# Performance work log

Hardware: AMD Instinct MI355X
Metric: run time of the kernel (lower is better)

The kernel has to match this reference:

```python
import jax, jax.numpy as jnp
import numpy as np

Q = 1024      # query length
R = 2048      # relative position length (2*Q, mems=None)
B = 2         # batch
D_MODEL = 1024
N_HEAD = 16
D_HEAD = 64
SCALE = 1.0 / (D_HEAD ** 0.5)
LN_EPS = 1e-12


def setup_inputs() -> dict:
    key = jax.random.key(0)
    ks = jax.random.split(key, 16)
    f32 = jnp.float32
    n = lambda k, s, sc=1.0: jax.random.normal(k, s, f32) * sc
    return {
        "h": n(ks[0], (Q, B, D_MODEL)),
        "r": n(ks[1], (R, B, D_MODEL)),
        "seg_mat": jax.random.randint(ks[2], (Q, Q, B), 0, 2).astype(bool),
        "attn_mask": jax.random.randint(ks[3], (Q, Q, B, 1), 0, 2).astype(f32),
        "q_kernel": n(ks[4], (D_MODEL, N_HEAD, D_HEAD), 0.02),
        "k_kernel": n(ks[5], (D_MODEL, N_HEAD, D_HEAD), 0.02),
        "v_kernel": n(ks[6], (D_MODEL, N_HEAD, D_HEAD), 0.02),
        "r_kernel": n(ks[7], (D_MODEL, N_HEAD, D_HEAD), 0.02),
        "o_kernel": n(ks[8], (D_MODEL, N_HEAD, D_HEAD), 0.02),
        "r_w_bias": n(ks[9], (N_HEAD, D_HEAD), 0.02),
        "r_r_bias": n(ks[10], (N_HEAD, D_HEAD), 0.02),
        "r_s_bias": n(ks[11], (N_HEAD, D_HEAD), 0.02),
        "seg_embed": n(ks[12], (2, N_HEAD, D_HEAD), 0.02),
        "ln_gamma": jnp.ones((D_MODEL,), f32),
        "ln_beta": jnp.zeros((D_MODEL,), f32),
    }


def _rel_shift(x, klen):
    # x: [q, rlen, b, n] -> [q, klen, b, n]
    q, rlen, b, n = x.shape
    x = x.reshape(rlen, q, b, n)[1:]
    x = x.reshape(q, rlen - 1, b, n)[:, :klen]
    return x


def _layer_norm(x, gamma, beta):
    mu = jnp.mean(x, axis=-1, keepdims=True)
    var = jnp.mean(jnp.square(x - mu), axis=-1, keepdims=True)
    return (x - mu) * jax.lax.rsqrt(var + LN_EPS) * gamma + beta


def reference(h, r, seg_mat, attn_mask, q_kernel, k_kernel, v_kernel,
              r_kernel, o_kernel, r_w_bias, r_r_bias, r_s_bias, seg_embed,
              ln_gamma, ln_beta):
    # projections (mems=None -> cat == h)
    q_head = jnp.einsum('ibh,hnd->ibnd', h, q_kernel)
    k_head = jnp.einsum('ibh,hnd->ibnd', h, k_kernel)
    v_head = jnp.einsum('ibh,hnd->ibnd', h, v_kernel)
    k_head_r = jnp.einsum('ibh,hnd->ibnd', r, r_kernel)

    klen = k_head.shape[0]
    # content score
    ac = jnp.einsum('ibnd,jbnd->ijbn', q_head + r_w_bias, k_head)
    # relative-position score with rel_shift
    bd = jnp.einsum('ibnd,jbnd->ijbn', q_head + r_r_bias, k_head_r)
    bd = _rel_shift(bd, klen)
    # segment bias: ef [q, 2, b, n] -> select per (i,j,b) via seg_mat
    ef = jnp.einsum('ibnd,snd->isbn', q_head + r_s_bias, seg_embed)
    ef = jnp.where(seg_mat[:, :, :, None], ef[:, 1:, :, :], ef[:, :1, :, :])

    attn_score = (ac + bd + ef) * SCALE
    attn_score = attn_score - 1e30 * attn_mask
    attn_prob = jax.nn.softmax(attn_score, axis=1)  # over key axis j

    attn_vec = jnp.einsum('ijbn,jbnd->ibnd', attn_prob, v_head)
    output = jnp.einsum('ibnd,hnd->ibh', attn_vec, o_kernel)
    return _layer_norm(output + h, ln_gamma, ln_beta)
```

## Files before the change

### kernel.cpp

```cpp
#include <hip/hip_runtime.h>

typedef __bf16 bf16x8 __attribute__((ext_vector_type(8)));
typedef float f32x4 __attribute__((ext_vector_type(4)));
typedef unsigned short us4 __attribute__((ext_vector_type(4)));

__device__ __forceinline__ unsigned short f2bf(float f) {
  unsigned int u = __builtin_bit_cast(unsigned int, f);
  u += 0x7fffu + ((u >> 16) & 1u);
  return (unsigned short)(u >> 16);
}
__device__ __forceinline__ float bf2f(unsigned short s) {
  unsigned int u = ((unsigned int)s) << 16;
  return __builtin_bit_cast(float, u);
}
__device__ __forceinline__ f32x4 mfma16(bf16x8 a, bf16x8 b, f32x4 c) {
  return __builtin_amdgcn_mfma_f32_16x16x32_bf16(a, b, c, 0, 0, 0);
}
__device__ __forceinline__ void gload16(const void* g, void* l) {
  __builtin_amdgcn_global_load_lds(
      (const __attribute__((address_space(1))) unsigned int*)g,
      (__attribute__((address_space(3))) unsigned int*)l, 16, 0, 0);
}
template <int CTRL>
__device__ __forceinline__ float dppf(float x) {
  return __builtin_bit_cast(
      float, __builtin_amdgcn_mov_dpp(__builtin_bit_cast(int, x), CTRL, 0xf, 0xf, true));
}
__device__ __forceinline__ float rmax16(float x) {
  x = fmaxf(x, dppf<0xB1>(x));
  x = fmaxf(x, dppf<0x4E>(x));
  x = fmaxf(x, dppf<0x124>(x));
  x = fmaxf(x, dppf<0x128>(x));
  return x;
}
__device__ __forceinline__ float rsum16(float x) {
  x += dppf<0xB1>(x);
  x += dppf<0x4E>(x);
  x += dppf<0x124>(x);
  x += dppf<0x128>(x);
  return x;
}

__global__ __launch_bounds__(256) void cast3_kernel(
    const float* __restrict__ h, const float* __restrict__ r, const float* __restrict__ wo,
    unsigned short* __restrict__ hb, unsigned short* __restrict__ rb,
    unsigned short* __restrict__ wo_b) {
  int idx = blockIdx.x * 256 + threadIdx.x;
  const float* in;
  unsigned short* out;
  int o;
  if (idx < 524288) { in = h; out = hb; o = idx; }
  else if (idx < 1572864) { in = r; out = rb; o = idx - 524288; }
  else { in = wo; out = wo_b; o = idx - 1572864; }
  float4 v = ((const float4*)in)[o];
  us4 t;
  t[0] = f2bf(v.x); t[1] = f2bf(v.y); t[2] = f2bf(v.z); t[3] = f2bf(v.w);
  *(us4*)&out[o * 4] = t;
}

__global__ __launch_bounds__(256) void transpose_cast4(
    const float* __restrict__ w0, const float* __restrict__ w1,
    const float* __restrict__ w2, const float* __restrict__ w3,
    unsigned short* __restrict__ o0, unsigned short* __restrict__ o1,
    unsigned short* __restrict__ o2, unsigned short* __restrict__ o3) {
  __shared__ float t[32][33];
  const int z = blockIdx.z;
  const float* in = z == 0 ? w0 : (z == 1 ? w1 : (z == 2 ? w2 : w3));
  unsigned short* out = z == 0 ? o0 : (z == 1 ? o1 : (z == 2 ? o2 : o3));
  int k0 = blockIdx.y * 32;
  int n0 = blockIdx.x * 32;
  int r = threadIdx.x >> 5;
  int c = threadIdx.x & 31;
#pragma unroll
  for (int s = 0; s < 4; ++s)
    t[r + s * 8][c] = in[(k0 + r + s * 8) * 1024 + n0 + c];
  __syncthreads();
#pragma unroll
  for (int s = 0; s < 4; ++s)
    out[(n0 + r + s * 8) * 1024 + k0 + c] = f2bf(t[c][r + s * 8]);
}

__global__ __launch_bounds__(256) void segmask_kernel(const unsigned char* __restrict__ seg,
                                                      const float* __restrict__ mask,
                                                      unsigned int* __restrict__ out) {
  int ij = blockIdx.x * 256 + threadIdx.x;
  unsigned short sv = *(const unsigned short*)&seg[ij * 2];
  float2 mv = *(const float2*)&mask[(size_t)ij * 2];
  unsigned int o0 = ((unsigned int)f2bf(mv.x * -1e30f) << 16) | ((sv & 0xffu) ? 0x3f80u : 0u);
  unsigned int o1 = ((unsigned int)f2bf(mv.y * -1e30f) << 16) | ((sv >> 8) ? 0x3f80u : 0u);
  out[ij] = o0;
  out[1048576 + ij] = o1;
}

__global__ __launch_bounds__(512) void proj4_kernel(
    const unsigned short* __restrict__ hb, const unsigned short* __restrict__ rb,
    const unsigned short* __restrict__ wq_t, const unsigned short* __restrict__ wk_t,
    const unsigned short* __restrict__ wv_t, const unsigned short* __restrict__ wr_t,
    const float* __restrict__ rwb, const float* __restrict__ rrb, const float* __restrict__ rsb,
    unsigned short* __restrict__ qwb, unsigned short* __restrict__ qrb,
    unsigned short* __restrict__ qsb,
    unsigned short* __restrict__ khb, unsigned short* __restrict__ vhb,
    unsigned short* __restrict__ krhb) {
  __shared__ unsigned short sA[2][128 * 64];
  __shared__ unsigned short sB[2][128 * 64];
  const int bx = blockIdx.x;
  int sel, rblk;
  const unsigned short* A;
  if (bx < 384) { sel = bx >> 7; rblk = bx & 127; A = hb; }
  else { sel = 3; rblk = bx - 384; A = rb; }
  const unsigned short* Bt = sel == 0 ? wq_t : (sel == 1 ? wk_t : (sel == 2 ? wv_t : wr_t));
  const int n0 = (rblk & 7) * 128, m0 = (rblk >> 3) * 128;
  const int tid = threadIdx.x, lane = tid & 63, w = tid >> 6;
  const int wm = w >> 1, wn = w & 1, g = lane >> 4, lc = lane & 15;

  f32x4 acc[2][4] = {};

  auto STAGE = [&](int buf, int kt) {
#pragma unroll
    for (int s = 0; s < 2; ++s) {
      int c = s * 512 + tid;
      int row = c >> 3;
      int ko = ((c & 7) ^ (row & 7)) * 8;
      int lbase = (s * 512 + w * 64) * 8;
      gload16(&A[(size_t)(m0 + row) * 1024 + kt + ko], &sA[buf][lbase]);
      gload16(&Bt[(size_t)(n0 + row) * 1024 + kt + ko], &sB[buf][lbase]);
    }
  };

  STAGE(0, 0);
  __syncthreads();

  for (int kt = 0; kt < 1024; kt += 64) {
    const int cur = (kt >> 6) & 1;
    if (kt < 960) STAGE(cur ^ 1, kt + 64);
    bf16x8 af[2][2], bfr[4][2];
#pragma unroll
    for (int ks = 0; ks < 2; ++ks) {
#pragma unroll
      for (int mi = 0; mi < 2; ++mi) {
        int ra = wm * 32 + mi * 16 + lc;
        af[mi][ks] = *(const bf16x8*)&sA[cur][ra * 64 + (((ks * 4 + g) ^ (ra & 7)) * 8)];
      }
#pragma unroll
      for (int ni = 0; ni < 4; ++ni) {
        int rb_ = wn * 64 + ni * 16 + lc;
        bfr[ni][ks] = *(const bf16x8*)&sB[cur][rb_ * 64 + (((ks * 4 + g) ^ (rb_ & 7)) * 8)];
      }
    }
#pragma unroll
    for (int ks = 0; ks < 2; ++ks)
#pragma unroll
      for (int mi = 0; mi < 2; ++mi)
#pragma unroll
        for (int ni = 0; ni < 4; ++ni)
          acc[mi][ni] = mfma16(af[mi][ks], bfr[ni][ks], acc[mi][ni]);
    __syncthreads();
  }

#pragma unroll
  for (int ni = 0; ni < 4; ++ni) {
    int col = n0 + wn * 64 + ni * 16 + lc;
    float bw = 0.f, br = 0.f, bs = 0.f;
    if (sel == 0) { bw = rwb[col]; br = rrb[col]; bs = rsb[col]; }
#pragma unroll
    for (int mi = 0; mi < 2; ++mi) {
      int rowb = m0 + wm * 32 + mi * 16 + g * 4;
#pragma unroll
      for (int r = 0; r < 4; ++r) {
        float v = acc[mi][ni][r];
        size_t idx = (size_t)(rowb + r) * 1024 + col;
        if (sel == 0) {
          qwb[idx] = f2bf((v + bw) * 0.125f);
          qrb[idx] = f2bf((v + br) * 0.125f);
          qsb[idx] = f2bf((v + bs) * 0.125f);
        } else if (sel == 1) {
          khb[idx] = f2bf(v);
        } else if (sel == 2) {
          vhb[idx] = f2bf(v);
        } else {
          krhb[idx] = f2bf(v);
        }
      }
    }
  }
}

__global__ __launch_bounds__(512) void gemm64_out(const unsigned short* __restrict__ A,
                                                  const unsigned short* __restrict__ Bt,
                                                  float* __restrict__ C) {
  __shared__ unsigned short sA[2][64 * 64];
  __shared__ unsigned short sB[2][128 * 64];
  const int tid = threadIdx.x, lane = tid & 63, w = tid >> 6;
  const int wm = w >> 2, wn = w & 3, g = lane >> 4, lc = lane & 15;
  const int m0 = blockIdx.y * 64, n0 = blockIdx.x * 128;
  f32x4 acc[2][2] = {};

  auto STAGE = [&](int buf, int kt) {
    {
      int c = tid;
      int row = c >> 3;
      int ko = ((c & 7) ^ (row & 7)) * 8;
      gload16(&A[(size_t)(m0 + row) * 1024 + kt + ko], &sA[buf][w * 64 * 8]);
    }
#pragma unroll
    for (int s = 0; s < 2; ++s) {
      int c = s * 512 + tid;
      int row = c >> 3;
      int ko = ((c & 7) ^ (row & 7)) * 8;
      gload16(&Bt[(size_t)(n0 + row) * 1024 + kt + ko], &sB[buf][(s * 512 + w * 64) * 8]);
    }
  };

  STAGE(0, 0);
  __syncthreads();

  for (int kt = 0; kt < 1024; kt += 64) {
    const int cur = (kt >> 6) & 1;
    if (kt < 960) STAGE(cur ^ 1, kt + 64);
    bf16x8 af[2][2], bfr[2][2];
#pragma unroll
    for (int ks = 0; ks < 2; ++ks) {
#pragma unroll
      for (int mi = 0; mi < 2; ++mi) {
        int ra = wm * 32 + mi * 16 + lc;
        af[mi][ks] = *(const bf16x8*)&sA[cur][ra * 64 + (((ks * 4 + g) ^ (ra & 7)) * 8)];
      }
#pragma unroll
      for (int ni = 0; ni < 2; ++ni) {
        int rb_ = wn * 32 + ni * 16 + lc;
        bfr[ni][ks] = *(const bf16x8*)&sB[cur][rb_ * 64 + (((ks * 4 + g) ^ (rb_ & 7)) * 8)];
      }
    }
#pragma unroll
    for (int ks = 0; ks < 2; ++ks)
#pragma unroll
      for (int mi = 0; mi < 2; ++mi)
#pragma unroll
        for (int ni = 0; ni < 2; ++ni)
          acc[mi][ni] = mfma16(af[mi][ks], bfr[ni][ks], acc[mi][ni]);
    __syncthreads();
  }
#pragma unroll
  for (int ni = 0; ni < 2; ++ni) {
    int col = n0 + wn * 32 + ni * 16 + lc;
#pragma unroll
    for (int mi = 0; mi < 2; ++mi) {
      int rowb = m0 + wm * 32 + mi * 16 + g * 4;
#pragma unroll
      for (int r = 0; r < 4; ++r)
        C[(size_t)(rowb + r) * 1024 + col] = acc[mi][ni][r];
    }
  }
}

__global__ __launch_bounds__(256) void transpose_v(const unsigned short* __restrict__ vh,
                                                   unsigned short* __restrict__ vT) {
  __shared__ unsigned short t[64][65];
  const int bn = blockIdx.y, j0 = blockIdx.x * 64;
  const int b = bn >> 4, n = bn & 15;
  const int r = threadIdx.x >> 4;
  const int c4 = (threadIdx.x & 15) * 4;
#pragma unroll
  for (int s = 0; s < 4; ++s) {
    int j = r + s * 16;
    us4 v = *(const us4*)&vh[((size_t)(j0 + j) * 2 + b) * 1024 + n * 64 + c4];
    t[j][c4 + 0] = v[0]; t[j][c4 + 1] = v[1]; t[j][c4 + 2] = v[2]; t[j][c4 + 3] = v[3];
  }
  __syncthreads();
#pragma unroll
  for (int s = 0; s < 4; ++s) {
    int d = r + s * 16;
    us4 v;
    v[0] = t[c4 + 0][d]; v[1] = t[c4 + 1][d]; v[2] = t[c4 + 2][d]; v[3] = t[c4 + 3][d];
    *(us4*)&vT[((size_t)bn * 64 + d) * 1024 + j0 + c4] = v;
  }
}

__global__ __launch_bounds__(256) void ef_kernel(const unsigned short* __restrict__ qs,
                                                 const float* __restrict__ seg_embed,
                                                 float* __restrict__ ef0, float* __restrict__ ef1) {
  int gw = blockIdx.x * 4 + (threadIdx.x >> 6);
  int lane = threadIdx.x & 63;
  int n = gw & 15, ib = gw >> 4;
  int i = ib >> 1, b = ib & 1;
  float qv = bf2f(qs[(size_t)ib * 1024 + n * 64 + lane]);
  float p0 = qv * seg_embed[n * 64 + lane];
  float p1 = qv * seg_embed[1024 + n * 64 + lane];
#pragma unroll
  for (int m = 1; m < 64; m <<= 1) {
    p0 += __shfl_xor(p0, m);
    p1 += __shfl_xor(p1, m);
  }
  if (lane == 0) {
    ef0[(b * 16 + n) * 1024 + i] = p0;
    ef1[(b * 16 + n) * 1024 + i] = p1;
  }
}

__global__ __launch_bounds__(512, 4) void attn_kernel(
    const unsigned short* __restrict__ qw, const unsigned short* __restrict__ qr,
    const unsigned short* __restrict__ kh, const unsigned short* __restrict__ krh,
    const unsigned short* __restrict__ vT,
    const float* __restrict__ ef0, const float* __restrict__ ef1,
    const unsigned int* __restrict__ segmask,
    float* __restrict__ part, float* __restrict__ ml) {
  __shared__ unsigned short sK[64][72];
  __shared__ unsigned short sVT[64][72];
  __shared__ unsigned short sKR[256][72];
  __shared__ unsigned short sP[8][16][80];

  const int tid = threadIdx.x, lane = tid & 63, w = tid >> 6;
  const int g = lane >> 4, lc = lane & 15;
  const int bn = blockIdx.x, b = bn >> 4, n = bn & 15;
  const int i0 = blockIdx.y * 128;
  const int js = blockIdx.z;
  const int S0 = 1024 + js * 512 - i0 - 127;

  bf16x8 fqw[2], fqr[2];
  const int qrow = i0 + w * 16 + lc;
#pragma unroll
  for (int ks = 0; ks < 2; ++ks) {
    size_t off = ((size_t)qrow * 2 + b) * 1024 + n * 64 + ks * 32 + g * 8;
    fqw[ks] = *(const bf16x8*)&qw[off];
    fqr[ks] = *(const bf16x8*)&qr[off];
  }
  float ef0v[4], dv[4];
  unsigned int smoff[4];
#pragma unroll
  for (int r = 0; r < 4; ++r) {
    int i = i0 + w * 16 + g * 4 + r;
    float e0 = ef0[bn * 1024 + i];
    ef0v[r] = e0;
    dv[r] = ef1[bn * 1024 + i] - e0;
    smoff[r] = ((unsigned)b << 20) | ((unsigned)i << 10) | (unsigned)lc;
  }
  float mrun[4], lsum[4];
  f32x4 accO[4] = {};
#pragma unroll
  for (int r = 0; r < 4; ++r) { mrun[r] = -3e38f; lsum[r] = 0.f; }

  const int srow = tid >> 3;
  const int sko = (tid & 7) * 8;

#pragma unroll
  for (int pp = 0; pp < 3; ++pp) {
    int jr = S0 + pp * 64 + srow;
    *(uint4*)&sKR[jr & 255][sko] =
        *(const uint4*)&krh[((size_t)jr * 2 + b) * 1024 + n * 64 + sko];
  }
  int j0 = js * 512;
  uint4 rK = *(const uint4*)&kh[((size_t)(j0 + srow) * 2 + b) * 1024 + n * 64 + sko];
  uint4 rV = *(const uint4*)&vT[((size_t)bn * 64 + srow) * 1024 + j0 + sko];
  uint4 rR = *(const uint4*)&krh[((size_t)(S0 + 192 + srow) * 2 + b) * 1024 + n * 64 + sko];

  for (int t = 0; t < 8; ++t) {
    j0 = (js * 8 + t) * 64;
    __syncthreads();
    *(uint4*)&sK[srow][sko] = rK;
    *(uint4*)&sVT[srow][sko] = rV;
    if (t < 7) {
      *(uint4*)&sKR[(S0 + 192 + t * 64 + srow) & 255][sko] = rR;
      int j0n = j0 + 64;
      rK = *(const uint4*)&kh[((size_t)(j0n + srow) * 2 + b) * 1024 + n * 64 + sko];
      rV = *(const uint4*)&vT[((size_t)bn * 64 + srow) * 1024 + j0n + sko];
      if (t < 6) {
        int jr = S0 + 256 + t * 64 + srow;
        if (jr > 2047) jr = 2047;
        rR = *(const uint4*)&krh[((size_t)jr * 2 + b) * 1024 + n * 64 + sko];
      }
    }
    unsigned int msv[4][4];
#pragma unroll
    for (int r = 0; r < 4; ++r)
#pragma unroll
      for (int nf = 0; nf < 4; ++nf)
        msv[r][nf] = segmask[smoff[r] + j0 + nf * 16];
    __syncthreads();

    const int base = S0 + t * 64 + (7 - w) * 16;
    f32x4 bdk[5];
#pragma unroll
    for (int k = 0; k < 5; ++k) {
      f32x4 a = {0.f, 0.f, 0.f, 0.f};
#pragma unroll
      for (int ks = 0; ks < 2; ++ks) {
        bf16x8 fk = *(const bf16x8*)&sKR[(base + k * 16 + lc) & 255][ks * 32 + g * 8];
        a = mfma16(fqr[ks], fk, a);
      }
      bdk[k] = a;
    }
    float p[4][4];
#pragma unroll
    for (int r = 0; r < 4; ++r) {
      const int a_ = g * 4 + r;
      const int srcl = (lane & 48) | ((lc + 15 - a_) & 15);
      float s0 = __shfl(bdk[0][r], srcl);
      float s1 = __shfl(bdk[1][r], srcl);
      float s2 = __shfl(bdk[2][r], srcl);
      float s3 = __shfl(bdk[3][r], srcl);
      float s4 = __shfl(bdk[4][r], srcl);
      const bool lo = lc <= a_;
#pragma unroll
      for (int nf = 0; nf < 4; ++nf) {
        unsigned int u = msv[r][nf];
        float sgv = bf2f((unsigned short)(u & 0xffffu));
        float mkv = bf2f((unsigned short)(u >> 16));
        float bdv = lo ? (nf == 0 ? s0 : nf == 1 ? s1 : nf == 2 ? s2 : s3)
                       : (nf == 0 ? s1 : nf == 1 ? s2 : nf == 2 ? s3 : s4);
        p[r][nf] = ef0v[r] + sgv * dv[r] + mkv + bdv;
      }
    }
    f32x4 aa[4];
#pragma unroll
    for (int nf = 0; nf < 4; ++nf) {
      f32x4 a = {0.f, 0.f, 0.f, 0.f};
#pragma unroll
      for (int ks = 0; ks < 2; ++ks) {
        bf16x8 fk = *(const bf16x8*)&sK[nf * 16 + lc][ks * 32 + g * 8];
        a = mfma16(fqw[ks], fk, a);
      }
      aa[nf] = a;
    }
#pragma unroll
    for (int r = 0; r < 4; ++r)
#pragma unroll
      for (int nf = 0; nf < 4; ++nf) p[r][nf] += aa[nf][r];

#pragma unroll
    for (int r = 0; r < 4; ++r) {
      float mt = fmaxf(fmaxf(p[r][0], p[r][1]), fmaxf(p[r][2], p[r][3]));
      mt = rmax16(mt);
      float mnew = fmaxf(mrun[r], mt);
      float corr = __expf(mrun[r] - mnew);
      mrun[r] = mnew;
      float se = 0.f;
#pragma unroll
      for (int nf = 0; nf < 4; ++nf) {
        float e = __expf(p[r][nf] - mnew);
        p[r][nf] = e;
        se += e;
      }
      se = rsum16(se);
      lsum[r] = lsum[r] * corr + se;
#pragma unroll
      for (int df = 0; df < 4; ++df) accO[df][r] *= corr;
#pragma unroll
      for (int nf = 0; nf < 4; ++nf)
        sP[w][g * 4 + r][nf * 16 + lc] = f2bf(p[r][nf]);
    }
#pragma unroll
    for (int ks = 0; ks < 2; ++ks) {
      bf16x8 fp = *(const bf16x8*)&sP[w][lc][ks * 32 + g * 8];
#pragma unroll
      for (int df = 0; df < 4; ++df) {
        bf16x8 fv = *(const bf16x8*)&sVT[df * 16 + lc][ks * 32 + g * 8];
        accO[df] = mfma16(fp, fv, accO[df]);
      }
    }
  }
#pragma unroll
  for (int r = 0; r < 4; ++r) {
    int i = i0 + w * 16 + g * 4 + r;
    size_t pb = ((size_t)(js * 32 + bn) * 1024 + i) * 64;
#pragma unroll
    for (int df = 0; df < 4; ++df) part[pb + df * 16 + lc] = accO[df][r];
    if (lc == 0) {
      size_t mb = (((size_t)js * 32 + bn) * 1024 + i) * 2;
      ml[mb] = mrun[r];
      ml[mb + 1] = lsum[r];
    }
  }
}

__global__ __launch_bounds__(256) void combine_kernel(const float* __restrict__ part,
                                                      const float* __restrict__ ml,
                                                      unsigned short* __restrict__ av) {
  int gw = blockIdx.x * 4 + (threadIdx.x >> 6);
  int lane = threadIdx.x & 63;
  int bn = gw >> 10, i = gw & 1023;
  int b = bn >> 4, n = bn & 15;
  float m0 = ml[((size_t)bn * 1024 + i) * 2];
  float l0 = ml[((size_t)bn * 1024 + i) * 2 + 1];
  float m1 = ml[(((size_t)32 + bn) * 1024 + i) * 2];
  float l1 = ml[(((size_t)32 + bn) * 1024 + i) * 2 + 1];
  float mx = fmaxf(m0, m1);
  float w0 = __expf(m0 - mx), w1 = __expf(m1 - mx);
  float inv = 1.f / (l0 * w0 + l1 * w1);
  float o = part[((size_t)bn * 1024 + i) * 64 + lane] * w0 +
            part[(((size_t)32 + bn) * 1024 + i) * 64 + lane] * w1;
  av[((size_t)i * 2 + b) * 1024 + n * 64 + lane] = f2bf(o * inv);
}

__global__ __launch_bounds__(256) void ln_kernel(const float* __restrict__ gout,
                                                 const float* __restrict__ h,
                                                 const float* __restrict__ gamma,
                                                 const float* __restrict__ beta,
                                                 float* __restrict__ out) {
  __shared__ float red[8];
  const int row = blockIdx.x;
  const int tid = threadIdx.x;
  float x[4];
  float s = 0.f;
#pragma unroll
  for (int q = 0; q < 4; ++q) {
    int d = tid + q * 256;
    x[q] = gout[(size_t)row * 1024 + d] + h[(size_t)row * 1024 + d];
    s += x[q];
  }
#pragma unroll
  for (int m = 1; m < 64; m <<= 1) s += __shfl_xor(s, m);
  if ((tid & 63) == 0) red[tid >> 6] = s;
  __syncthreads();
  s = red[0] + red[1] + red[2] + red[3];
  float mu = s * (1.f / 1024.f);
  float v = 0.f;
#pragma unroll
  for (int q = 0; q < 4; ++q) {
    float dd = x[q] - mu;
    v += dd * dd;
  }
#pragma unroll
  for (int m = 1; m < 64; m <<= 1) v += __shfl_xor(v, m);
  if ((tid & 63) == 0) red[4 + (tid >> 6)] = v;
  __syncthreads();
  v = red[4] + red[5] + red[6] + red[7];
  float rstd = rsqrtf(v * (1.f / 1024.f) + 1e-12f);
#pragma unroll
  for (int q = 0; q < 4; ++q) {
    int d = tid + q * 256;
    out[(size_t)row * 1024 + d] = (x[q] - mu) * rstd * gamma[d] + beta[d];
  }
}

extern "C" void kernel_launch(void* const* d_in, const int* in_sizes, int n_in,
                              void* d_out, int out_size, void* d_ws, size_t ws_size,
                              hipStream_t stream) {
  const float* h = (const float*)d_in[0];
  const float* r = (const float*)d_in[1];
  const unsigned char* seg = (const unsigned char*)d_in[2];
  const float* mask = (const float*)d_in[3];
  const float* wq = (const float*)d_in[4];
  const float* wk = (const float*)d_in[5];
  const float* wv = (const float*)d_in[6];
  const float* wr = (const float*)d_in[7];
  const float* wo = (const float*)d_in[8];
  const float* rwb = (const float*)d_in[9];
  const float* rrb = (const float*)d_in[10];
  const float* rsb = (const float*)d_in[11];
  const float* seg_embed = (const float*)d_in[12];
  const float* gamma = (const float*)d_in[13];
  const float* beta = (const float*)d_in[14];
  float* out = (float*)d_out;

  char* ws = (char*)d_ws;
  size_t off = 0;
  auto alloc = [&](size_t bytes) {
    size_t cur = off;
    off = (off + bytes + 255) & ~(size_t)255;
    return cur;
  };
  unsigned short* hb = (unsigned short*)(ws + alloc(2048 * 1024 * 2));
  unsigned short* rb = (unsigned short*)(ws + alloc(4096 * 1024 * 2));
  unsigned short* wq_t = (unsigned short*)(ws + alloc(1024 * 1024 * 2));
  unsigned short* wk_t = (unsigned short*)(ws + alloc(1024 * 1024 * 2));
  unsigned short* wv_t = (unsigned short*)(ws + alloc(1024 * 1024 * 2));
  unsigned short* wr_t = (unsigned short*)(ws + alloc(1024 * 1024 * 2));
  unsigned short* wo_b = (unsigned short*)(ws + alloc(1024 * 1024 * 2));
  unsigned short* qwb = (unsigned short*)(ws + alloc(2048 * 1024 * 2));
  unsigned short* qrb = (unsigned short*)(ws + alloc(2048 * 1024 * 2));
  unsigned short* qsb = (unsigned short*)(ws + alloc(2048 * 1024 * 2));
  unsigned short* khb = (unsigned short*)(ws + alloc(2048 * 1024 * 2));
  unsigned short* vhb = (unsigned short*)(ws + alloc(2048 * 1024 * 2));
  unsigned short* krhb = (unsigned short*)(ws + alloc(4096 * 1024 * 2));
  unsigned short* vTb = (unsigned short*)(ws + alloc(2048 * 1024 * 2));
  float* ef0 = (float*)(ws + alloc(2048 * 16 * 4));
  float* ef1 = (float*)(ws + alloc(2048 * 16 * 4));
  unsigned int* segmask = (unsigned int*)(ws + alloc(2 * 1024 * 1024 * 4));
  unsigned short* avb = (unsigned short*)(ws + alloc(2048 * 1024 * 2));
  float* gout = (float*)(ws + alloc(2048 * 1024 * 4));
  float* part = (float*)(ws + alloc((size_t)2 * 32 * 1024 * 64 * 4));
  float* mlb = (float*)(ws + alloc((size_t)2 * 32 * 1024 * 2 * 4));
  (void)ws_size; (void)in_sizes; (void)n_in; (void)out_size;

  cast3_kernel<<<7168, 256, 0, stream>>>(h, r, wo, hb, rb, wo_b);
  transpose_cast4<<<dim3(32, 32, 4), 256, 0, stream>>>(wq, wk, wv, wr, wq_t, wk_t, wv_t, wr_t);
  segmask_kernel<<<4096, 256, 0, stream>>>(seg, mask, segmask);

  proj4_kernel<<<640, 512, 0, stream>>>(hb, rb, wq_t, wk_t, wv_t, wr_t, rwb, rrb, rsb,
                                        qwb, qrb, qsb, khb, vhb, krhb);

  transpose_v<<<dim3(16, 32), 256, 0, stream>>>(vhb, vTb);
  ef_kernel<<<8192, 256, 0, stream>>>(qsb, seg_embed, ef0, ef1);

  attn_kernel<<<dim3(32, 8, 2), 512, 0, stream>>>(qwb, qrb, khb, krhb, vTb,
                                                  ef0, ef1, segmask, part, mlb);
  combine_kernel<<<8192, 256, 0, stream>>>(part, mlb, avb);

  gemm64_out<<<dim3(8, 32), 512, 0, stream>>>(avb, wo_b, gout);
  ln_kernel<<<2048, 256, 0, stream>>>(gout, h, gamma, beta, out);
}
```

Baseline: 143.1 us.

## Deepen projection GEMM pipeline to four K=32 stages with vmcnt-based waits

Replaces the double-buffered K=64 staging in the projection GEMM with a 4-slot ring of K=32 tiles, keeping three loads in flight. Waits use explicit s_waitcnt vmcnt counts plus a raw barrier instead of __syncthreads. The LDS swizzle is adapted to the 32-wide rows, and MFMA issue priority is raised around the compute. The aim is to hide global-to-LDS latency better, at the cost of more barriers per K step and hand-managed counters that must exactly match the number of outstanding loads.

```diff
diff --git a/kernel.cpp b/kernel.cpp
--- a/kernel.cpp
+++ b/kernel.cpp
@@ -101,8 +101,8 @@
     unsigned short* __restrict__ qsb,
     unsigned short* __restrict__ khb, unsigned short* __restrict__ vhb,
     unsigned short* __restrict__ krhb) {
-  __shared__ unsigned short sA[2][128 * 64];
-  __shared__ unsigned short sB[2][128 * 64];
+  __shared__ unsigned short sA[4][128 * 32];
+  __shared__ unsigned short sB[4][128 * 32];
   const int bx = blockIdx.x;
   int sel, rblk;
   const unsigned short* A;
@@ -115,47 +115,56 @@
 
   f32x4 acc[2][4] = {};
 
-  auto STAGE = [&](int buf, int kt) {
-#pragma unroll
-    for (int s = 0; s < 2; ++s) {
-      int c = s * 512 + tid;
-      int row = c >> 3;
-      int ko = ((c & 7) ^ (row & 7)) * 8;
-      int lbase = (s * 512 + w * 64) * 8;
-      gload16(&A[(size_t)(m0 + row) * 1024 + kt + ko], &sA[buf][lbase]);
-      gload16(&Bt[(size_t)(n0 + row) * 1024 + kt + ko], &sB[buf][lbase]);
-    }
+  const int srow = tid >> 2;
+  const int sslot = tid & 3;
+  const int sko = (sslot ^ ((srow >> 1) & 3)) * 8;
+  const unsigned short* aptr = &A[(size_t)(m0 + srow) * 1024 + sko];
+  const unsigned short* bptr = &Bt[(size_t)(n0 + srow) * 1024 + sko];
+  const int ldst = w * 64 * 8;
+
+  auto STAGE = [&](int slot, int kt) {
+    gload16(aptr + kt, &sA[slot][ldst]);
+    gload16(bptr + kt, &sB[slot][ldst]);
   };
+  auto COMPUTE = [&](int slot) {
+    bf16x8 af[2], bfr[4];
+#pragma unroll
+    for (int mi = 0; mi < 2; ++mi) {
+      int ra = wm * 32 + mi * 16 + lc;
+      af[mi] = *(const bf16x8*)&sA[slot][ra * 32 + ((g ^ ((ra >> 1) & 3)) * 8)];
+    }
+#pragma unroll
+    for (int ni = 0; ni < 4; ++ni) {
+      int rb_ = wn * 64 + ni * 16 + lc;
+      bfr[ni] = *(const bf16x8*)&sB[slot][rb_ * 32 + ((g ^ ((rb_ >> 1) & 3)) * 8)];
+    }
+    __builtin_amdgcn_s_setprio(1);
+#pragma unroll
+    for (int mi = 0; mi < 2; ++mi)
+#pragma unroll
+      for (int ni = 0; ni < 4; ++ni)
+        acc[mi][ni] = mfma16(af[mi], bfr[ni], acc[mi][ni]);
+    __builtin_amdgcn_s_setprio(0);
+  };
 
   STAGE(0, 0);
-  __syncthreads();
-
-  for (int kt = 0; kt < 1024; kt += 64) {
-    const int cur = (kt >> 6) & 1;
-    if (kt < 960) STAGE(cur ^ 1, kt + 64);
-    bf16x8 af[2][2], bfr[4][2];
-#pragma unroll
-    for (int ks = 0; ks < 2; ++ks) {
-#pragma unroll
-      for (int mi = 0; mi < 2; ++mi) {
-        int ra = wm * 32 + mi * 16 + lc;
-        af[mi][ks] = *(const bf16x8*)&sA[cur][ra * 64 + (((ks * 4 + g) ^ (ra & 7)) * 8)];
-      }
-#pragma unroll
-      for (int ni = 0; ni < 4; ++ni) {
-        int rb_ = wn * 64 + ni * 16 + lc;
-        bfr[ni][ks] = *(const bf16x8*)&sB[cur][rb_ * 64 + (((ks * 4 + g) ^ (rb_ & 7)) * 8)];
-      }
-    }
-#pragma unroll
-    for (int ks = 0; ks < 2; ++ks)
-#pragma unroll
-      for (int mi = 0; mi < 2; ++mi)
-#pragma unroll
-        for (int ni = 0; ni < 4; ++ni)
-          acc[mi][ni] = mfma16(af[mi][ks], bfr[ni][ks], acc[mi][ni]);
-    __syncthreads();
-  }
+  STAGE(1, 32);
+  STAGE(2, 64);
+  for (int s = 0; s < 30; ++s) {
+    asm volatile("s_waitcnt vmcnt(4)" ::: "memory");
+    __builtin_amdgcn_s_barrier();
+    asm volatile("" ::: "memory");
+    if (s < 29) STAGE((s + 3) & 3, (s + 3) * 32);
+    COMPUTE(s & 3);
+  }
+  asm volatile("s_waitcnt vmcnt(2)" ::: "memory");
+  __builtin_amdgcn_s_barrier();
+  asm volatile("" ::: "memory");
+  COMPUTE(2);
+  asm volatile("s_waitcnt vmcnt(0)" ::: "memory");
+  __builtin_amdgcn_s_barrier();
+  asm volatile("" ::: "memory");
+  COMPUTE(3);
 
 #pragma unroll
   for (int ni = 0; ni < 4; ++ni) {
```

Result: faster. 140.0 us (-2.2%).
